# Optimization experiments

Hardware: AMD Instinct MI355X
Metric: run time of the kernel (lower is better)

## Reference

```python
import jax, jax.numpy as jnp
import numpy as np

N_PATCH = 676
K_SEL = int(676 * 0.8)  # 540
HEADS = 16
LN_EPS = 1e-5


def _layernorm(t, w, b):
    mu = t.mean(-1, keepdims=True)
    var = ((t - mu) ** 2).mean(-1, keepdims=True)
    return (t - mu) * jax.lax.rsqrt(var + LN_EPS) * w + b


def _attention(t, w_qkv, b_qkv, w_out, b_out):
    # t: [S, B, C] (seq-first, like torch nn.MultiheadAttention)
    S, B, C = t.shape
    D = C // HEADS
    qkv = t @ w_qkv.T + b_qkv                       # [S, B, 3C]
    q, k, v = jnp.split(qkv, 3, axis=-1)
    def heads(a):
        return a.reshape(S, B, HEADS, D).transpose(1, 2, 0, 3)  # [B,H,S,D]
    q, k, v = heads(q), heads(k), heads(v)
    scores = jnp.einsum('bhqd,bhkd->bhqk', q, k) / jnp.sqrt(jnp.asarray(D, t.dtype))
    attn = jax.nn.softmax(scores, axis=-1)
    o = jnp.einsum('bhqk,bhkd->bhqd', attn, v)      # [B,H,S,D]
    o = o.transpose(2, 0, 1, 3).reshape(S, B, C)
    return o @ w_out.T + b_out


def _mlp(t, w_fc1, b_fc1, w_fc2, b_fc2):
    h = t @ w_fc1.T + b_fc1
    h = h * jax.nn.sigmoid(1.702 * h)  # CLIP QuickGELU
    return h @ w_fc2.T + b_fc2


def setup_inputs() -> dict:
    key = jax.random.key(0)
    ks = jax.random.split(key, 6)
    C, B, L = 1024, 32, 77
    inp = {
        'x': jax.random.normal(ks[0], (1 + N_PATCH, B, C), jnp.float32),
        'lang_tokens': jax.random.normal(ks[1], (L, B, C), jnp.float32),
        'ln1_w': jnp.ones((C,), jnp.float32),
        'ln1_b': jnp.zeros((C,), jnp.float32),
        'ln2_w': jnp.ones((C,), jnp.float32),
        'ln2_b': jnp.zeros((C,), jnp.float32),
        'w_qkv': jax.random.normal(ks[2], (3 * C, C), jnp.float32) * 0.02,
        'b_qkv': jnp.zeros((3 * C,), jnp.float32),
        'w_out': jax.random.normal(ks[3], (C, C), jnp.float32) * 0.02,
        'b_out': jnp.zeros((C,), jnp.float32),
        'w_fc1': jax.random.normal(ks[4], (4 * C, C), jnp.float32) * 0.02,
        'b_fc1': jnp.zeros((4 * C,), jnp.float32),
        'w_fc2': jax.random.normal(ks[5], (C, 4 * C), jnp.float32) * 0.02,
        'b_fc2': jnp.zeros((C,), jnp.float32),
    }
    return inp


def reference(x, lang_tokens, ln1_w, ln1_b, ln2_w, ln2_b, w_qkv, b_qkv,
              w_out, b_out, w_fc1, b_fc1, w_fc2, b_fc2):
    Nfull, B, C = x.shape
    cls_x = x[:1]            # [1, B, C]
    xt = x[1:]               # [676, B, C]

    # per-token language-alignment score: [676, B]
    score = jnp.einsum('nbc,lbc->nbl', xt, lang_tokens).mean(-1)

    # top-k selection per batch column; torch boolean-mask gather preserves
    # the ORIGINAL token order within the high/low sets -> sort the indices.
    order = jnp.argsort(-score, axis=0)                 # descending
    high_idx = jnp.sort(order[:K_SEL], axis=0)          # [540, B]
    low_idx = jnp.sort(order[K_SEL:], axis=0)           # [136, B]

    delta_x = jnp.take_along_axis(xt, high_idx[:, :, None], axis=0)  # [540,B,C]
    low_x = jnp.take_along_axis(xt, low_idx[:, :, None], axis=0)     # [136,B,C]
    low_score = jnp.take_along_axis(score, low_idx, axis=0)[:, :, None]
    low_tok = (low_x * jax.nn.softmax(low_score, axis=0)).sum(0, keepdims=True)

    seq = jnp.concatenate([cls_x, delta_x, low_tok], axis=0)  # [542, B, C]
    d = _attention(_layernorm(seq, ln1_w, ln1_b), w_qkv, b_qkv, w_out, b_out)

    barange = jnp.arange(B)[None, :]
    temple = jnp.zeros_like(xt)
    temple = temple.at[high_idx, barange].set(d[1:-1])
    temple = temple.at[low_idx, barange].set(
        jnp.broadcast_to(d[-1:], (N_PATCH - K_SEL, B, C)))

    xt = xt + temple
    cls_x = cls_x + d[:1]
    x = jnp.concatenate([cls_x, xt], axis=0)
    x = x + _mlp(_layernorm(x, ln2_w, ln2_b), w_fc1, b_fc1, w_fc2, b_fc2)
    return x
```

## Files before the change

### kernel.cpp

```cpp
#include <hip/hip_runtime.h>
#include <hip/hip_bf16.h>

typedef unsigned short u16;
typedef __attribute__((ext_vector_type(4))) float f32x4;
typedef __attribute__((ext_vector_type(8))) short s16x8;

#define DEVI __device__ __forceinline__

static constexpr int NPATCH = 676;
static constexpr int KSEL   = 540;
static constexpr int NLOW   = 136;
static constexpr int BB     = 32;
static constexpr int CC     = 1024;
static constexpr int S      = 542;
static constexpr int SP     = 576;
static constexpr int M1P    = SP * BB;
static constexpr int NTOK   = 677;
static constexpr int M2     = NTOK * BB;
static constexpr int M2P    = 21760;
static constexpr int NKT    = SP / 64;
static constexpr int NQC    = 5;

DEVI u16 f2bf(float f) {
  unsigned u = __float_as_uint(f);
  u += 0x7fffu + ((u >> 16) & 1u);
  return (u16)(u >> 16);
}
DEVI float bf2f(u16 h) { return __uint_as_float(((unsigned)h) << 16); }
DEVI float ex2(float x) { float r; asm("v_exp_f32 %0, %1" : "=v"(r) : "v"(x)); return r; }

DEVI void gld16(const void* g, void* l) {
  __builtin_amdgcn_global_load_lds((const __attribute__((address_space(1))) void*)g,
                                   (__attribute__((address_space(3))) void*)l,
                                   16, 0, 0);
}

DEVI void BAR() {
  asm volatile("" ::: "memory");
  __builtin_amdgcn_s_barrier();
  asm volatile("" ::: "memory");
}
#define VMC(N) asm volatile("s_waitcnt vmcnt(" #N ")" ::: "memory")


__global__ void k_f2bf4(const float* __restrict__ in, u16* __restrict__ out, int n4) {
  int i = blockIdx.x * blockDim.x + threadIdx.x;
  if (i >= n4) return;
  float4 v = ((const float4*)in)[i];
  unsigned long long p = (unsigned long long)f2bf(v.x)
                       | ((unsigned long long)f2bf(v.y) << 16)
                       | ((unsigned long long)f2bf(v.z) << 32)
                       | ((unsigned long long)f2bf(v.w) << 48);
  *(unsigned long long*)&out[(long)i * 4] = p;
}

__global__ void k_langmean(const float* __restrict__ lang, float* __restrict__ lm) {
  int b = blockIdx.x, t = threadIdx.x;
  float a0 = 0, a1 = 0, a2 = 0, a3 = 0;
  for (int l = 0; l < 77; l++) {
    float4 v = ((const float4*)(lang + ((long)l * BB + b) * CC))[t];
    a0 += v.x; a1 += v.y; a2 += v.z; a3 += v.w;
  }
  const float inv = 1.f / 77.f;
  float4 o; o.x = a0 * inv; o.y = a1 * inv; o.z = a2 * inv; o.w = a3 * inv;
  ((float4*)(lm + b * CC))[t] = o;
}

__global__ void k_score(const float* __restrict__ x, const float* __restrict__ lm,
                        float* __restrict__ score) {
  int nb = blockIdx.x;
  int n = nb >> 5, b = nb & 31;
  int t = threadIdx.x;
  float4 xv = ((const float4*)(x + ((long)(n + 1) * BB + b) * CC))[t];
  float4 lv = ((const float4*)(lm + b * CC))[t];
  float s = xv.x * lv.x + xv.y * lv.y + xv.z * lv.z + xv.w * lv.w;
  for (int m = 1; m < 64; m <<= 1) s += __shfl_xor(s, m);
  __shared__ float sm[4];
  if ((t & 63) == 0) sm[t >> 6] = s;
  __syncthreads();
  if (t == 0) score[n * BB + b] = sm[0] + sm[1] + sm[2] + sm[3];
}

__global__ void k_select(const float* __restrict__ score, float* __restrict__ wall,
                         int* __restrict__ rowmap, int* __restrict__ selsrc,
                         int* __restrict__ lowlist) {
  int b = blockIdx.x, t = threadIdx.x;
  __shared__ float sc[NPATCH];
  __shared__ int hf[NPATCH];
  __shared__ float red[2];
  if (t < NPATCH) sc[t] = score[t * BB + b];
  __syncthreads();
  int high = 0;
  if (t < NPATCH) {
    float s = sc[t];
    int r = 0;
    for (int m = 0; m < NPATCH; m++) {
      float sm_ = sc[m];
      r += (sm_ > s) || (sm_ == s && m < t);
    }
    high = (r < KSEL);
    hf[t] = high;
  }
  __syncthreads();
  if (t < NPATCH) {
    int p = 0;
    for (int m = 0; m < t; m++) p += hf[m];
    if (high) {
      rowmap[b * NPATCH + t] = 1 + p;
      selsrc[b * S + 1 + p] = t + 1;
    } else {
      rowmap[b * NPATCH + t] = S - 1;
      lowlist[b * NLOW + (t - p)] = t;
    }
  }
  if (t == 0) selsrc[b * S + 0] = 0;
  __syncthreads();
  if (t == 0) {
    float m = -3e38f;
    for (int i = 0; i < NPATCH; i++) if (!hf[i]) m = fmaxf(m, sc[i]);
    float d = 0;
    for (int i = 0; i < NPATCH; i++) if (!hf[i]) d += __expf(sc[i] - m);
    red[0] = m; red[1] = d;
  }
  __syncthreads();
  if (t < NPATCH) wall[b * NPATCH + t] = hf[t] ? 0.f : __expf(sc[t] - red[0]) / red[1];
}

__global__ void k_lowtok(const float* __restrict__ x, const float* __restrict__ wall,
                         const int* __restrict__ lowlist, float* __restrict__ lowtok) {
  int b = blockIdx.x, ch = blockIdx.y;
  int c = ch * 256 + threadIdx.x;
  float acc = 0.f;
  for (int i = 0; i < NLOW; i++) {
    int n = lowlist[b * NLOW + i];
    acc += wall[b * NPATCH + n] * x[((long)(n + 1) * BB + b) * CC + c];
  }
  lowtok[b * CC + c] = acc;
}

__global__ void k_lnseq(const float* __restrict__ x, const float* __restrict__ lowtok,
                        const int* __restrict__ selsrc, const float* __restrict__ w,
                        const float* __restrict__ bias, u16* __restrict__ out) {
  int s = blockIdx.x, b = blockIdx.y, t = threadIdx.x;
  u16* orow = out + ((long)b * SP + s) * CC;
  if (s >= S) { *(unsigned long long*)&orow[4 * t] = 0ULL; return; }
  const float* src;
  if (s == 0)          src = x + (long)b * CC;
  else if (s == S - 1) src = lowtok + (long)b * CC;
  else                 src = x + ((long)selsrc[b * S + s] * BB + b) * CC;
  float4 v = ((const float4*)src)[t];
  float ss = v.x + v.y + v.z + v.w;
  float s2 = v.x * v.x + v.y * v.y + v.z * v.z + v.w * v.w;
  for (int k = 1; k < 64; k <<= 1) { ss += __shfl_xor(ss, k); s2 += __shfl_xor(s2, k); }
  __shared__ float sa[4], sb[4];
  if ((t & 63) == 0) { sa[t >> 6] = ss; sb[t >> 6] = s2; }
  __syncthreads();
  ss = sa[0] + sa[1] + sa[2] + sa[3];
  s2 = sb[0] + sb[1] + sb[2] + sb[3];
  float mu = ss * (1.f / CC);
  float var = s2 * (1.f / CC) - mu * mu;
  float rs = rsqrtf(var + 1e-5f);
  int c = 4 * t;
  unsigned long long p = (unsigned long long)f2bf((v.x - mu) * rs * w[c]     + bias[c])
                       | ((unsigned long long)f2bf((v.y - mu) * rs * w[c + 1] + bias[c + 1]) << 16)
                       | ((unsigned long long)f2bf((v.z - mu) * rs * w[c + 2] + bias[c + 2]) << 32)
                       | ((unsigned long long)f2bf((v.w - mu) * rs * w[c + 3] + bias[c + 3]) << 48);
  *(unsigned long long*)&orow[4 * t] = p;
}

__global__ void k_scatln(const float* __restrict__ x, const u16* __restrict__ dbuf,
                         const int* __restrict__ rowmap, const float* __restrict__ w,
                         const float* __restrict__ bias, float* __restrict__ out,
                         u16* __restrict__ lnout) {
  int m = blockIdx.x, t = threadIdx.x;
  u16* orow = lnout + (long)m * CC;
  if (m >= M2) { *(unsigned long long*)&orow[4 * t] = 0ULL; return; }
  int nf = m >> 5, b = m & 31;
  int srow = (nf == 0) ? 0 : rowmap[b * NPATCH + (nf - 1)];
  float4 xv = ((const float4*)(x + (long)m * CC))[t];
  unsigned long long dp = *(const unsigned long long*)&dbuf[((long)b * SP + srow) * CC + 4 * t];
  float4 v;
  v.x = xv.x + bf2f((u16)(dp));
  v.y = xv.y + bf2f((u16)(dp >> 16));
  v.z = xv.z + bf2f((u16)(dp >> 32));
  v.w = xv.w + bf2f((u16)(dp >> 48));
  ((float4*)(out + (long)m * CC))[t] = v;
  float ss = v.x + v.y + v.z + v.w;
  float s2 = v.x * v.x + v.y * v.y + v.z * v.z + v.w * v.w;
  for (int k = 1; k < 64; k <<= 1) { ss += __shfl_xor(ss, k); s2 += __shfl_xor(s2, k); }
  __shared__ float sa[4], sb[4];
  if ((t & 63) == 0) { sa[t >> 6] = ss; sb[t >> 6] = s2; }
  __syncthreads();
  ss = sa[0] + sa[1] + sa[2] + sa[3];
  s2 = sb[0] + sb[1] + sb[2] + sb[3];
  float mu = ss * (1.f / CC);
  float var = s2 * (1.f / CC) - mu * mu;
  float rs = rsqrtf(var + 1e-5f);
  int c = 4 * t;
  unsigned long long p = (unsigned long long)f2bf((v.x - mu) * rs * w[c]     + bias[c])
                       | ((unsigned long long)f2bf((v.y - mu) * rs * w[c + 1] + bias[c + 1]) << 16)
                       | ((unsigned long long)f2bf((v.z - mu) * rs * w[c + 2] + bias[c + 2]) << 32)
                       | ((unsigned long long)f2bf((v.w - mu) * rs * w[c + 3] + bias[c + 3]) << 48);
  *(unsigned long long*)&orow[4 * t] = p;
}


struct Epi {
  const float* bias;
  u16* obf;
  float* of;
  u16 *qb, *kb, *vtb;
  int mvalid, ldc;
};

DEVI void stage32(u16* dst, const u16* src, int ld) {
  int t = threadIdx.x;
#pragma unroll
  for (int q = 0; q < 2; q++) {
    int s = t + q * 256;
    int R = s >> 3, clp = s & 7;
    int lc = clp ^ (R & 7);
    int m = 2 * R + (lc >> 2), kc = lc & 3;
    gld16(src + (long)m * ld + kc * 8, dst + s * 8);
  }
}

DEVI s16x8 frag32(const u16* tile, int m, int h4) {
  int R = m >> 1;
  int phys = ((((m & 1) << 2) | h4) ^ (R & 7));
  return *(const s16x8*)(tile + R * 64 + phys * 8);
}

DEVI void stage64(u16* dst, const u16* src, int ld) {
  int t = threadIdx.x;
  int c = t & 7, r0 = t >> 3;
  gld16(src + (long)r0 * ld + ((c ^ (r0 & 7)) << 3), dst + t * 8);
  int r1 = r0 + 32;
  gld16(src + (long)r1 * ld + ((c ^ (r1 & 7)) << 3), dst + 2048 + t * 8);
}

DEVI s16x8 frag(const u16* half, int rh, int kk, int h4) {
  int chunk = ((kk << 2) | h4) ^ (rh & 7);
  return *(const s16x8*)(half + rh * 64 + chunk * 8);
}

template<int MODE>
__global__ __launch_bounds__(256, 4) void k_gemm3(const u16* __restrict__ A, int lda,
                                                  const u16* __restrict__ Bw, int ldb,
                                                  int K, Epi e) {
  __shared__ __align__(16) u16 lds[2][2][4096];
  int t = threadIdx.x;
  int lane = t & 63, w = t >> 6;
  int h4 = lane >> 4, r = lane & 15;
  int wr = w >> 1, wc = w & 1;
  int MBk = gridDim.x, NBk = gridDim.y;
  int nwg = MBk * NBk;
  int orig = blockIdx.y * MBk + blockIdx.x;
  int q8 = nwg >> 3, r8 = nwg & 7, xcd = orig & 7, rk = orig >> 3;
  int wgid = (xcd < r8 ? xcd * (q8 + 1) : r8 * (q8 + 1) + (xcd - r8) * q8) + rk;
  int bm = wgid / NBk, bn = wgid % NBk;

  const u16* Asrc = A + (long)bm * 128 * lda;
  const u16* Bsrc = Bw + (long)bn * 128 * ldb;
  int NT = K >> 5;

  f32x4 acc[4][4];
#pragma unroll
  for (int i = 0; i < 4; i++)
#pragma unroll
    for (int j = 0; j < 4; j++) acc[i][j] = {0.f, 0.f, 0.f, 0.f};

  stage32(lds[0][0], Asrc, lda);
  stage32(lds[0][1], Bsrc, ldb);
  __syncthreads();

  for (int kt = 0; kt < NT; kt++) {
    int cur = kt & 1;
    if (kt + 1 < NT) {
      stage32(lds[cur ^ 1][0], Asrc + (kt + 1) * 32, lda);
      stage32(lds[cur ^ 1][1], Bsrc + (kt + 1) * 32, ldb);
    }
    const u16* At = lds[cur][0];
    const u16* Bt = lds[cur][1];
    s16x8 af[4], bf[4];
#pragma unroll
    for (int i = 0; i < 4; i++) af[i] = frag32(At, wr * 64 + i * 16 + r, h4);
#pragma unroll
    for (int j = 0; j < 4; j++) bf[j] = frag32(Bt, wc * 64 + j * 16 + r, h4);
#pragma unroll
    for (int i = 0; i < 4; i++)
#pragma unroll
      for (int j = 0; j < 4; j++)
        acc[i][j] = __builtin_amdgcn_mfma_f32_16x16x32_bf16(af[i], bf[j], acc[i][j], 0, 0, 0);
    __syncthreads();
  }

  const float QSC = 0.125f * 1.44269504088896f;
#pragma unroll
  for (int i = 0; i < 4; i++) {
    int m0 = bm * 128 + wr * 64 + i * 16 + 4 * h4;
#pragma unroll
    for (int j = 0; j < 4; j++) {
      int n = bn * 128 + wc * 64 + j * 16 + r;
      float bias = (MODE == 3 && e.bias == nullptr) ? 0.f : e.bias[n];
      if (MODE == 0) {
        int part = n >> 10, cc = n & 1023;
        int hh = cc >> 6, dd = cc & 63;
        int b0 = m0 / SP, s0 = m0 % SP;
        if (part == 2) {
          u16 pk[4];
#pragma unroll
          for (int tt = 0; tt < 4; tt++) pk[tt] = f2bf(acc[i][j][tt] + bias);
          *(unsigned long long*)&e.vtb[((long)(b0 * 16 + hh) * 64 + dd) * SP + s0] =
              *(unsigned long long*)pk;
        } else {
          u16* dst = (part == 0 ? e.qb : e.kb) + ((long)(b0 * 16 + hh) * SP + s0) * 64 + dd;
          float scl = (part == 0) ? QSC : 1.f;
#pragma unroll
          for (int tt = 0; tt < 4; tt++) dst[tt * 64] = f2bf((acc[i][j][tt] + bias) * scl);
        }
      } else if (MODE == 1) {
#pragma unroll
        for (int tt = 0; tt < 4; tt++)
          e.obf[(long)(m0 + tt) * e.ldc + n] = f2bf(acc[i][j][tt] + bias);
      } else if (MODE == 2) {
#pragma unroll
        for (int tt = 0; tt < 4; tt++) {
          float v = acc[i][j][tt] + bias;
          v = v / (1.f + __expf(-1.702f * v));
          e.obf[(long)(m0 + tt) * e.ldc + n] = f2bf(v);
        }
      } else {
#pragma unroll
        for (int tt = 0; tt < 4; tt++) {
          int m = m0 + tt;
          if (m < e.mvalid) e.of[(long)m * CC + n] += acc[i][j][tt] + bias;
        }
      }
    }
  }
}


__global__ __launch_bounds__(256, 4) void k_attn2(const u16* __restrict__ qb,
                                                  const u16* __restrict__ kb,
                                                  const u16* __restrict__ vtb,
                                                  u16* __restrict__ aout) {
  __shared__ __align__(16) u16 Kt[2][4096];
  __shared__ __align__(16) u16 Vt[2][4096];
  __shared__ __align__(16) u16 Pl[4][1024];

  int nwg = gridDim.x;
  int orig = blockIdx.x;
  int q8 = nwg >> 3, r8 = nwg & 7, xcd = orig & 7, rk = orig >> 3;
  int wgid = (xcd < r8 ? xcd * (q8 + 1) : r8 * (q8 + 1) + (xcd - r8) * q8) + rk;
  int bh = wgid / NQC, qc = wgid % NQC;
  int b = bh >> 4, hh = bh & 15;
  int t = threadIdx.x, w = t >> 6, lane = t & 63;
  int h4 = lane >> 4, r = lane & 15;

  const u16* Q  = qb  + (long)bh * SP * 64;
  const u16* Kg = kb  + (long)bh * SP * 64;
  const u16* Vg = vtb + (long)bh * 64 * SP;

  int qt[2];
  bool act[2];
  s16x8 aq0[2], aq1[2];
  f32x4 o[2][4];
  float mM[2][4], lL[2][4];
#pragma unroll
  for (int sub = 0; sub < 2; sub++) {
    qt[sub] = qc * 8 + w * 2 + sub;
    act[sub] = qt[sub] < SP / 16;
    if (act[sub]) {
      aq0[sub] = *(const s16x8*)&Q[(qt[sub] * 16 + r) * 64 + h4 * 8];
      aq1[sub] = *(const s16x8*)&Q[(qt[sub] * 16 + r) * 64 + 32 + h4 * 8];
    }
#pragma unroll
    for (int i = 0; i < 4; i++) { o[sub][i] = {0.f, 0.f, 0.f, 0.f}; mM[sub][i] = -1e30f; lL[sub][i] = 0.f; }
  }

  stage64(Kt[0], Kg, 64);
  stage64(Vt[0], Vg, SP);
  VMC(0);
  BAR();

  for (int kt = 0; kt < NKT; kt++) {
    int cur = kt & 1;
    if (kt + 1 < NKT) {
      stage64(Kt[cur ^ 1], Kg + (kt + 1) * 64 * 64, 64);
      stage64(Vt[cur ^ 1], Vg + (kt + 1) * 64, SP);
    }
    int kv0 = kt * 64;
    const u16* Kc = Kt[cur];
    const u16* Vc = Vt[cur];
#pragma unroll
    for (int sub = 0; sub < 2; sub++) {
      if (!act[sub]) continue;
      f32x4 sf[4];
#pragma unroll
      for (int f = 0; f < 4; f++) {
        sf[f] = {0.f, 0.f, 0.f, 0.f};
        sf[f] = __builtin_amdgcn_mfma_f32_16x16x32_bf16(aq0[sub], frag(Kc, f * 16 + r, 0, h4), sf[f], 0, 0, 0);
        sf[f] = __builtin_amdgcn_mfma_f32_16x16x32_bf16(aq1[sub], frag(Kc, f * 16 + r, 1, h4), sf[f], 0, 0, 0);
      }
      if (kv0 + 64 > S) {
#pragma unroll
        for (int f = 0; f < 4; f++)
          if (kv0 + f * 16 + r >= S) {
#pragma unroll
            for (int tt = 0; tt < 4; tt++) sf[f][tt] = -1e30f;
          }
      }
      float mx[4];
#pragma unroll
      for (int tt = 0; tt < 4; tt++)
        mx[tt] = fmaxf(fmaxf(sf[0][tt], sf[1][tt]), fmaxf(sf[2][tt], sf[3][tt]));
      for (int msk = 1; msk < 16; msk <<= 1) {
#pragma unroll
        for (int tt = 0; tt < 4; tt++) mx[tt] = fmaxf(mx[tt], __shfl_xor(mx[tt], msk));
      }
      int need = 0;
#pragma unroll
      for (int tt = 0; tt < 4; tt++) need |= (mx[tt] > mM[sub][tt] + 8.f);
      if (__any(need)) {
#pragma unroll
        for (int tt = 0; tt < 4; tt++) {
          float mn = fmaxf(mM[sub][tt], mx[tt]);
          float sc = ex2(mM[sub][tt] - mn);
          mM[sub][tt] = mn;
          lL[sub][tt] *= sc;
#pragma unroll
          for (int nf = 0; nf < 4; nf++) o[sub][nf][tt] *= sc;
        }
      }
      float rs[4];
#pragma unroll
      for (int tt = 0; tt < 4; tt++) {
        float m_ = mM[sub][tt];
        float p0 = ex2(sf[0][tt] - m_), p1 = ex2(sf[1][tt] - m_);
        float p2 = ex2(sf[2][tt] - m_), p3 = ex2(sf[3][tt] - m_);
        sf[0][tt] = p0; sf[1][tt] = p1; sf[2][tt] = p2; sf[3][tt] = p3;
        rs[tt] = (p0 + p1) + (p2 + p3);
      }
      for (int msk = 1; msk < 16; msk <<= 1) {
#pragma unroll
        for (int tt = 0; tt < 4; tt++) rs[tt] += __shfl_xor(rs[tt], msk);
      }
#pragma unroll
      for (int tt = 0; tt < 4; tt++) lL[sub][tt] += rs[tt];
      u16* Pw = Pl[w];
#pragma unroll
      for (int f = 0; f < 4; f++)
#pragma unroll
        for (int tt = 0; tt < 4; tt++) {
          int q = 4 * h4 + tt;
          int chunk = (f * 2 + (r >> 3)) ^ (q & 7);
          Pw[q * 64 + chunk * 8 + (r & 7)] = f2bf(sf[f][tt]);
        }
      s16x8 pa0 = frag(Pw, r, 0, h4);
      s16x8 pa1 = frag(Pw, r, 1, h4);
#pragma unroll
      for (int nf = 0; nf < 4; nf++) {
        o[sub][nf] = __builtin_amdgcn_mfma_f32_16x16x32_bf16(pa0, frag(Vc, nf * 16 + r, 0, h4), o[sub][nf], 0, 0, 0);
        o[sub][nf] = __builtin_amdgcn_mfma_f32_16x16x32_bf16(pa1, frag(Vc, nf * 16 + r, 1, h4), o[sub][nf], 0, 0, 0);
      }
    }
    VMC(0);
    BAR();
  }

#pragma unroll
  for (int sub = 0; sub < 2; sub++) {
    if (!act[sub]) continue;
    float inv[4];
#pragma unroll
    for (int tt = 0; tt < 4; tt++) inv[tt] = 1.f / lL[sub][tt];
#pragma unroll
    for (int nf = 0; nf < 4; nf++)
#pragma unroll
      for (int tt = 0; tt < 4; tt++) {
        int q = qt[sub] * 16 + 4 * h4 + tt;
        if (q < S) aout[((long)b * SP + q) * CC + hh * 64 + nf * 16 + r] = f2bf(o[sub][nf][tt] * inv[tt]);
      }
  }
}


extern "C" void kernel_launch(void* const* d_in, const int* in_sizes, int n_in,
                              void* d_out, int out_size, void* d_ws, size_t ws_size,
                              hipStream_t stream) {
  const float* x    = (const float*)d_in[0];
  const float* lang = (const float*)d_in[1];
  const float* ln1w = (const float*)d_in[2];
  const float* ln1b = (const float*)d_in[3];
  const float* ln2w = (const float*)d_in[4];
  const float* ln2b = (const float*)d_in[5];
  const float* wqkv = (const float*)d_in[6];
  const float* bqkv = (const float*)d_in[7];
  const float* wout = (const float*)d_in[8];
  const float* bout = (const float*)d_in[9];
  const float* wfc1 = (const float*)d_in[10];
  const float* bfc1 = (const float*)d_in[11];
  const float* wfc2 = (const float*)d_in[12];
  const float* bfc2 = (const float*)d_in[13];
  float* out = (float*)d_out;
  char* ws = (char*)d_ws;
  const size_t MiB = 1ull << 20;

  float* lm      = (float*)(ws + 0 * MiB);
  float* score   = (float*)(ws + 1 * MiB);
  float* wall    = (float*)(ws + 2 * MiB);
  int*   rowmap  = (int*)  (ws + 3 * MiB);
  int*   selsrc  = (int*)  (ws + 4 * MiB);
  int*   lowlist = (int*)  (ws + 5 * MiB);
  float* lowtok  = (float*)(ws + 6 * MiB);
  u16* wqb  = (u16*)(ws + 7 * MiB);
  u16* wob  = (u16*)(ws + 13 * MiB);
  u16* wf1b = (u16*)(ws + 15 * MiB);
  u16* wf2b = (u16*)(ws + 23 * MiB);
  u16* qbuf = (u16*)(ws + 31 * MiB);
  u16* kbuf = (u16*)(ws + 67 * MiB);
  u16* vtb  = (u16*)(ws + 103 * MiB);
  u16* regA = (u16*)(ws + 139 * MiB);
  u16* lnseq = regA;
  u16* aout  = regA;
  u16* dbuf  = vtb;
  u16* ln2bf = qbuf;
  u16* hbuf  = (u16*)(ws + 74 * MiB);

  {
    int n4;
    n4 = 3072 * 1024 / 4; k_f2bf4<<<(n4 + 255) / 256, 256, 0, stream>>>(wqkv, wqb, n4);
    n4 = 1024 * 1024 / 4; k_f2bf4<<<(n4 + 255) / 256, 256, 0, stream>>>(wout, wob, n4);
    n4 = 4096 * 1024 / 4; k_f2bf4<<<(n4 + 255) / 256, 256, 0, stream>>>(wfc1, wf1b, n4);
    n4 = 1024 * 4096 / 4; k_f2bf4<<<(n4 + 255) / 256, 256, 0, stream>>>(wfc2, wf2b, n4);
  }

  k_langmean<<<BB, 256, 0, stream>>>(lang, lm);
  k_score<<<NPATCH * BB, 256, 0, stream>>>(x, lm, score);
  k_select<<<BB, 1024, 0, stream>>>(score, wall, rowmap, selsrc, lowlist);
  k_lowtok<<<dim3(BB, 4), 256, 0, stream>>>(x, wall, lowlist, lowtok);
  k_lnseq<<<dim3(SP, BB), 256, 0, stream>>>(x, lowtok, selsrc, ln1w, ln1b, lnseq);

  {
    Epi e = {};
    e.bias = bqkv; e.qb = qbuf; e.kb = kbuf; e.vtb = vtb; e.mvalid = M1P;
    k_gemm3<0><<<dim3(M1P / 128, 3072 / 128), 256, 0, stream>>>(lnseq, 1024, wqb, 1024, 1024, e);
  }

  k_attn2<<<BB * 16 * NQC, 256, 0, stream>>>(qbuf, kbuf, vtb, aout);

  {
    Epi e = {};
    e.bias = bout; e.obf = dbuf; e.mvalid = M1P; e.ldc = 1024;
    k_gemm3<1><<<dim3(M1P / 128, 1024 / 128), 256, 0, stream>>>(aout, 1024, wob, 1024, 1024, e);
  }

  k_scatln<<<M2P, 256, 0, stream>>>(x, dbuf, rowmap, ln2w, ln2b, out, ln2bf);

  for (int c = 0; c < 2; c++) {
    Epi e2 = {};
    e2.bias = bfc1 + c * 2048; e2.obf = hbuf; e2.mvalid = M2P; e2.ldc = 2048;
    k_gemm3<2><<<dim3(M2P / 128, 2048 / 128), 256, 0, stream>>>(ln2bf, 1024, wf1b + (long)c * 2048 * 1024, 1024, 1024, e2);
    Epi e3 = {};
    e3.bias = (c == 0 ? bfc2 : nullptr); e3.of = out; e3.mvalid = M2;
    k_gemm3<3><<<dim3(M2P / 128, 1024 / 128), 256, 0, stream>>>(hbuf, 2048, wf2b + c * 2048, 4096, 2048, e3);
  }
}
```

Measured before the change: 1.100 ms.

## Deepen GEMM K-loop pipeline to four LDS stages with prefetch distance two

Replaces the double-buffered GEMM main loop with a four-slot LDS ring that prefetches two K-tiles ahead, using explicit vmcnt waits and a single barrier per iteration instead of two __syncthreads. This is meant to hide global-load latency behind more MFMA work and cut barrier overhead. In exchange LDS per block doubles and launch bounds drop to two blocks per SM, which reduces occupancy.

Result: slower. 1.156 ms (+5.1%).

```diff
diff --git a/kernel.cpp b/kernel.cpp
--- a/kernel.cpp
+++ b/kernel.cpp
@@ -245,10 +245,10 @@
 }
 
 template<int MODE>
-__global__ __launch_bounds__(256, 4) void k_gemm3(const u16* __restrict__ A, int lda,
+__global__ __launch_bounds__(256, 2) void k_gemm4(const u16* __restrict__ A, int lda,
                                                   const u16* __restrict__ Bw, int ldb,
                                                   int K, Epi e) {
-  __shared__ __align__(16) u16 lds[2][2][4096];
+  __shared__ __align__(16) u16 lds[4][2][4096];
   int t = threadIdx.x;
   int lane = t & 63, w = t >> 6;
   int h4 = lane >> 4, r = lane & 15;
@@ -272,16 +272,24 @@
 
   stage32(lds[0][0], Asrc, lda);
   stage32(lds[0][1], Bsrc, ldb);
-  __syncthreads();
+  if (NT > 1) {
+    stage32(lds[1][0], Asrc + 32, lda);
+    stage32(lds[1][1], Bsrc + 32, ldb);
+  }
 
   for (int kt = 0; kt < NT; kt++) {
-    int cur = kt & 1;
-    if (kt + 1 < NT) {
-      stage32(lds[cur ^ 1][0], Asrc + (kt + 1) * 32, lda);
-      stage32(lds[cur ^ 1][1], Bsrc + (kt + 1) * 32, ldb);
-    }
-    const u16* At = lds[cur][0];
-    const u16* Bt = lds[cur][1];
+    if (kt + 2 < NT) {
+      stage32(lds[(kt + 2) & 3][0], Asrc + (kt + 2) * 32, lda);
+      stage32(lds[(kt + 2) & 3][1], Bsrc + (kt + 2) * 32, ldb);
+      VMC(8);
+    } else if (kt + 1 < NT) {
+      VMC(4);
+    } else {
+      VMC(0);
+    }
+    BAR();
+    const u16* At = lds[kt & 3][0];
+    const u16* Bt = lds[kt & 3][1];
     s16x8 af[4], bf[4];
 #pragma unroll
     for (int i = 0; i < 4; i++) af[i] = frag32(At, wr * 64 + i * 16 + r, h4);
@@ -292,7 +300,6 @@
 #pragma unroll
       for (int j = 0; j < 4; j++)
         acc[i][j] = __builtin_amdgcn_mfma_f32_16x16x32_bf16(af[i], bf[j], acc[i][j], 0, 0, 0);
-    __syncthreads();
   }
 
   const float QSC = 0.125f * 1.44269504088896f;
@@ -546,7 +553,7 @@
   {
     Epi e = {};
     e.bias = bqkv; e.qb = qbuf; e.kb = kbuf; e.vtb = vtb; e.mvalid = M1P;
-    k_gemm3<0><<<dim3(M1P / 128, 3072 / 128), 256, 0, stream>>>(lnseq, 1024, wqb, 1024, 1024, e);
+    k_gemm4<0><<<dim3(M1P / 128, 3072 / 128), 256, 0, stream>>>(lnseq, 1024, wqb, 1024, 1024, e);
   }
 
   k_attn2<<<BB * 16 * NQC, 256, 0, stream>>>(qbuf, kbuf, vtb, aout);
@@ -554,7 +561,7 @@
   {
     Epi e = {};
     e.bias = bout; e.obf = dbuf; e.mvalid = M1P; e.ldc = 1024;
-    k_gemm3<1><<<dim3(M1P / 128, 1024 / 128), 256, 0, stream>>>(aout, 1024, wob, 1024, 1024, e);
+    k_gemm4<1><<<dim3(M1P / 128, 1024 / 128), 256, 0, stream>>>(aout, 1024, wob, 1024, 1024, e);
   }
 
   k_scatln<<<M2P, 256, 0, stream>>>(x, dbuf, rowmap, ln2w, ln2b, out, ln2bf);
@@ -562,9 +569,9 @@
   for (int c = 0; c < 2; c++) {
     Epi e2 = {};
     e2.bias = bfc1 + c * 2048; e2.obf = hbuf; e2.mvalid = M2P; e2.ldc = 2048;
-    k_gemm3<2><<<dim3(M2P / 128, 2048 / 128), 256, 0, stream>>>(ln2bf, 1024, wf1b + (long)c * 2048 * 1024, 1024, 1024, e2);
+    k_gemm4<2><<<dim3(M2P / 128, 2048 / 128), 256, 0, stream>>>(ln2bf, 1024, wf1b + (long)c * 2048 * 1024, 1024, 1024, e2);
     Epi e3 = {};
     e3.bias = (c == 0 ? bfc2 : nullptr); e3.of = out; e3.mvalid = M2;
-    k_gemm3<3><<<dim3(M2P / 128, 1024 / 128), 256, 0, stream>>>(hbuf, 2048, wf2b + c * 2048, 4096, 2048, e3);
-  }
-}
+    k_gemm4<3><<<dim3(M2P / 128, 1024 / 128), 256, 0, stream>>>(hbuf, 2048, wf2b + c * 2048, 4096, 2048, e3);
+  }
+}
```
